# Performance work log

Hardware: AMD Instinct MI355X
Metric: run time of the kernel (lower is better)

Reference implementation:

```python
import jax, jax.numpy as jnp
import numpy as np

DIM = 512
NUM_HEADS = 8
HEAD_DIM = DIM // NUM_HEADS
EPS = 1e-6


def setup_inputs() -> dict:
    key = jax.random.key(0)
    k_x, k_qkv, k_out, k_b = jax.random.split(key, 4)
    B, N = 8, 4096
    x = jax.random.normal(k_x, (B, N, DIM), dtype=jnp.float32)
    # nn.Linear weights stored as [out_features, in_features]; we keep [in, out] for x @ W
    s_qkv = 1.0 / np.sqrt(DIM)
    W_qkv = jax.random.uniform(k_qkv, (DIM, 3 * DIM), minval=-s_qkv, maxval=s_qkv, dtype=jnp.float32)
    W_out = jax.random.uniform(k_out, (DIM, DIM), minval=-s_qkv, maxval=s_qkv, dtype=jnp.float32)
    b_out = jax.random.uniform(k_b, (DIM,), minval=-s_qkv, maxval=s_qkv, dtype=jnp.float32)
    return {"x": x, "W_qkv": W_qkv, "W_out": W_out, "b_out": b_out}


def _feature_map(x):
    # elu(x) + 1
    return jax.nn.elu(x) + 1.0


def reference(x, W_qkv, W_out, b_out):
    B, N, C = x.shape
    H, D = NUM_HEADS, HEAD_DIM
    qkv = x @ W_qkv                              # [B, N, 3C]
    qkv = qkv.reshape(B, N, 3, H, D).transpose(2, 0, 3, 1, 4)  # [3, B, H, N, D]
    q, k, v = qkv[0], qkv[1], qkv[2]
    q_phi = _feature_map(q)                      # [B, H, N, D]
    k_phi = _feature_map(k)
    KV = jnp.einsum('bhnd,bhne->bhde', k_phi, v)  # [B, H, D, D]
    K_sum = k_phi.sum(axis=2)                     # [B, H, D]
    denom = jnp.einsum('bhnd,bhd->bhn', q_phi, K_sum)[..., None] + EPS  # [B, H, N, 1]
    out = jnp.einsum('bhnd,bhde->bhne', q_phi, KV) / denom              # [B, H, N, D]
    out = out.transpose(0, 2, 1, 3).reshape(B, N, C)
    return out @ W_out + b_out
```

## Files before the change

### kernel.cpp

```cpp
#include <hip/hip_runtime.h>
#include <stdint.h>

typedef float    f32x4 __attribute__((ext_vector_type(4)));
typedef short    s16x8 __attribute__((ext_vector_type(8)));
typedef short    s16x4 __attribute__((ext_vector_type(4)));
typedef unsigned short u16;
typedef uint32_t u32;

#define DEVINL __device__ __forceinline__

DEVINL float bf2f(u16 u) { union { u32 i; float f; } x; x.i = ((u32)u) << 16; return x.f; }
DEVINL u16 f2bf(float f) {
  union { float f; u32 i; } x; x.f = f;
  u32 i = x.i;
  return (u16)((i + 0x7FFFu + ((i >> 16) & 1u)) >> 16);
}

DEVINL void gload16(const void* g, void* l) {
  __builtin_amdgcn_global_load_lds((const __attribute__((address_space(1))) void*)g,
                                   (__attribute__((address_space(3))) void*)l,
                                   16, 0, 0);
}

__global__ __launch_bounds__(256) void k_prep(const float* __restrict__ x,
                                              u16* __restrict__ xb,
                                              const float* __restrict__ Wqkv,
                                              u16* __restrict__ wqkvt,
                                              const float* __restrict__ Wout,
                                              u16* __restrict__ woutt) {
  __shared__ __align__(16) float t[64][65];
  int b = blockIdx.x;
  int tid = threadIdx.x;
  if (b < 2048) {
    const int n8 = 2097152;
    int stride = 2048 * 256;
    for (int i = b * 256 + tid; i < n8; i += stride) {
      const f32x4* p = (const f32x4*)(x + (size_t)i * 8);
      f32x4 a = p[0], c = p[1];
      s16x8 o;
      o[0] = (short)f2bf(a[0]); o[1] = (short)f2bf(a[1]);
      o[2] = (short)f2bf(a[2]); o[3] = (short)f2bf(a[3]);
      o[4] = (short)f2bf(c[0]); o[5] = (short)f2bf(c[1]);
      o[6] = (short)f2bf(c[2]); o[7] = (short)f2bf(c[3]);
      *(s16x8*)(xb + (size_t)i * 8) = o;
    }
    return;
  }
  const float* W; u16* Wt; int K, N, tb;
  if (b < 2048 + 192) { W = Wqkv; Wt = wqkvt; K = 512; N = 1536; tb = b - 2048; }
  else               { W = Wout; Wt = woutt; K = 512; N = 512;  tb = b - 2240; }
  int nb = N >> 6;
  int tn = tb % nb, tk = tb / nb;
  int n0 = tn << 6, k0 = tk << 6;
  int cr = tid >> 4, cc = (tid & 15) << 2;
#pragma unroll
  for (int i = 0; i < 4; i++) {
    int r = cr + (i << 4);
    f32x4 v = *(const f32x4*)(W + (size_t)(k0 + r) * N + n0 + cc);
    t[r][cc] = v[0]; t[r][cc + 1] = v[1]; t[r][cc + 2] = v[2]; t[r][cc + 3] = v[3];
  }
  __syncthreads();
#pragma unroll
  for (int i = 0; i < 4; i++) {
    int nn = cr + (i << 4);
    s16x4 o;
    o[0] = (short)f2bf(t[cc    ][nn]);
    o[1] = (short)f2bf(t[cc + 1][nn]);
    o[2] = (short)f2bf(t[cc + 2][nn]);
    o[3] = (short)f2bf(t[cc + 3][nn]);
    *(s16x4*)(Wt + (size_t)(n0 + nn) * K + k0 + cc) = o;
  }
}

__global__ __launch_bounds__(512, 1) void k_gemm1(
    const u16* __restrict__ A, const u16* __restrict__ Bt,
    u16* __restrict__ qph, u16* __restrict__ kphT, u16* __restrict__ vT) {
  __shared__ __align__(16) u16 lsA[3][256 * 32];
  __shared__ __align__(16) u16 lsB[3][256 * 32];
  const int nbn = 6;
  int nwg = gridDim.x;
  int bx = blockIdx.x;
  int o = (bx & 7) * (nwg >> 3) + (bx >> 3);
  int bm = o / nbn, bn = o % nbn;
  int m0 = bm << 8, n0 = bn << 8;
  int tid = threadIdx.x;
  int w = tid >> 6, lane = tid & 63;
  int lnlo = lane & 15, lnhi = lane >> 4;
  int wr = w >> 2, wc = w & 3;

  const u16* gAp[2]; const u16* gBp[2]; int ldst[2];
#pragma unroll
  for (int i = 0; i < 2; i++) {
    int c = tid + i * 512;
    int row = c >> 2, ch = c & 3;
    int gch = ch ^ ((row >> 1) & 3);
    gAp[i] = A + (size_t)(m0 + row) * 512 + gch * 8;
    gBp[i] = Bt + (size_t)(n0 + row) * 512 + gch * 8;
    ldst[i] = c * 8;
  }
  int offA[8], offB[4];
#pragma unroll
  for (int f = 0; f < 8; f++) {
    int r = wr * 128 + f * 16 + lnlo;
    offA[f] = r * 32 + (lnhi ^ ((r >> 1) & 3)) * 8;
  }
#pragma unroll
  for (int f = 0; f < 4; f++) {
    int r = wc * 64 + f * 16 + lnlo;
    offB[f] = r * 32 + (lnhi ^ ((r >> 1) & 3)) * 8;
  }

  f32x4 acc[8][4] = {};

#pragma unroll
  for (int i = 0; i < 2; i++) gload16(gAp[i], &lsA[0][ldst[i]]);
#pragma unroll
  for (int i = 0; i < 2; i++) gload16(gBp[i], &lsB[0][ldst[i]]);
#pragma unroll
  for (int i = 0; i < 2; i++) gload16(gAp[i] + 32, &lsA[1][ldst[i]]);
#pragma unroll
  for (int i = 0; i < 2; i++) gload16(gBp[i] + 32, &lsB[1][ldst[i]]);
  asm volatile("s_waitcnt vmcnt(4)" ::: "memory");
  __builtin_amdgcn_s_barrier();

#pragma unroll
  for (int t = 0; t < 16; t++) {
    int buf = t % 3;
    const u16* La = &lsA[buf][0];
    const u16* Lb = &lsB[buf][0];
    int k2 = (t + 2) * 32;
    int b2 = (t + 2) % 3;

    s16x8 bf[4], af[4];
#pragma unroll
    for (int f = 0; f < 4; f++) bf[f] = *(const s16x8*)(Lb + offB[f]);
#pragma unroll
    for (int f = 0; f < 4; f++) af[f] = *(const s16x8*)(La + offA[f]);
    if (t < 14) {
#pragma unroll
      for (int i = 0; i < 2; i++) gload16(gAp[i] + k2, &lsA[b2][ldst[i]]);
    }
    __builtin_amdgcn_s_barrier();
    __builtin_amdgcn_s_setprio(1);
#pragma unroll
    for (int mf = 0; mf < 4; mf++)
#pragma unroll
      for (int nf = 0; nf < 4; nf++)
        acc[mf][nf] = __builtin_amdgcn_mfma_f32_16x16x32_bf16(af[mf], bf[nf], acc[mf][nf], 0, 0, 0);
    __builtin_amdgcn_s_setprio(0);
    __builtin_amdgcn_s_barrier();

    s16x8 af2[4];
#pragma unroll
    for (int f = 0; f < 4; f++) af2[f] = *(const s16x8*)(La + offA[4 + f]);
    if (t < 14) {
#pragma unroll
      for (int i = 0; i < 2; i++) gload16(gBp[i] + k2, &lsB[b2][ldst[i]]);
    }
    __builtin_amdgcn_s_barrier();
    __builtin_amdgcn_s_setprio(1);
#pragma unroll
    for (int mf = 0; mf < 4; mf++)
#pragma unroll
      for (int nf = 0; nf < 4; nf++)
        acc[4 + mf][nf] = __builtin_amdgcn_mfma_f32_16x16x32_bf16(af2[mf], bf[nf], acc[4 + mf][nf], 0, 0, 0);
    __builtin_amdgcn_s_setprio(0);
    if (t <= 13)      asm volatile("s_waitcnt vmcnt(4)" ::: "memory");
    else if (t == 14) asm volatile("s_waitcnt vmcnt(0)" ::: "memory");
    if (t < 15) __builtin_amdgcn_s_barrier();
  }

  int gmB = m0 + wr * 128;
  int gnB = n0 + wc * 64;
  int sec = n0 >> 9;
  if (sec == 0) {
#pragma unroll
    for (int mf = 0; mf < 8; mf++) {
#pragma unroll
      for (int nf = 0; nf < 4; nf++) {
        int col = gnB + nf * 16 + lnlo;
        int hh = (col >> 6) & 7;
        int dd = col & 63;
#pragma unroll
        for (int r = 0; r < 4; r++) {
          int rowm = gmB + mf * 16 + lnhi * 4 + r;
          float val = acc[mf][nf][r];
          val = (val > 0.f) ? (val + 1.f) : __expf(val);
          int bidx = rowm >> 12, tok = rowm & 4095;
          qph[(((size_t)(bidx * 8 + hh) * 4096 + tok) << 6) + dd] = f2bf(val);
        }
      }
    }
  } else {
    u16* dstT = (sec == 1) ? kphT : vT;
    bool isphi = (sec == 1);
#pragma unroll
    for (int mf = 0; mf < 8; mf++) {
      int rowm = gmB + mf * 16 + lnhi * 4;
      int bidx = rowm >> 12, tok = rowm & 4095;
#pragma unroll
      for (int nf = 0; nf < 4; nf++) {
        int col = gnB + nf * 16 + lnlo;
        int hh = (col >> 6) & 7;
        int dd = col & 63;
        s16x4 o4;
#pragma unroll
        for (int r = 0; r < 4; r++) {
          float val = acc[mf][nf][r];
          if (isphi) val = (val > 0.f) ? (val + 1.f) : __expf(val);
          o4[r] = (short)f2bf(val);
        }
        *(s16x4*)&dstT[((size_t)(bidx * 8 + hh) * 64 + dd) * 4096 + tok] = o4;
      }
    }
  }
}

__global__ __launch_bounds__(256, 2) void k_kv(const u16* __restrict__ kphT,
                                               const u16* __restrict__ vT,
                                               float* __restrict__ kvpart,
                                               float* __restrict__ kspart) {
  __shared__ __align__(16) u16 lsK[64 * 256];
  __shared__ __align__(16) u16 lsV[64 * 256];
  __shared__ float red[4][64];
  int bx = blockIdx.x;
  int bh = bx >> 4, ck = bx & 15;
  int tid = threadIdx.x, w = tid >> 6, lane = tid & 63;
  int lnlo = lane & 15, lnhi = lane >> 4;
  size_t gbase = (size_t)bh * 64 * 4096 + ck * 256;

#pragma unroll
  for (int i = 0; i < 8; i++) {
    int c = tid + i * 256;
    int row = c >> 5, ch = c & 31;
    int gch = ch ^ (row & 31);
    gload16(kphT + gbase + (size_t)row * 4096 + gch * 8, &lsK[c * 8]);
  }
#pragma unroll
  for (int i = 0; i < 8; i++) {
    int c = tid + i * 256;
    int row = c >> 5, ch = c & 31;
    int gch = ch ^ (row & 31);
    gload16(vT + gbase + (size_t)row * 4096 + gch * 8, &lsV[c * 8]);
  }
  asm volatile("s_waitcnt vmcnt(0)" ::: "memory");
  __builtin_amdgcn_s_barrier();

  f32x4 acc[4] = {{0.f, 0.f, 0.f, 0.f}, {0.f, 0.f, 0.f, 0.f},
                  {0.f, 0.f, 0.f, 0.f}, {0.f, 0.f, 0.f, 0.f}};
  int rb = w * 16 + lnlo;
#pragma unroll
  for (int kk = 0; kk < 8; kk++) {
    s16x8 bfr = *(const s16x8*)&lsV[rb * 256 + ((kk * 4 + lnhi) ^ (rb & 31)) * 8];
#pragma unroll
    for (int mf = 0; mf < 4; mf++) {
      int ra = mf * 16 + lnlo;
      s16x8 af = *(const s16x8*)&lsK[ra * 256 + ((kk * 4 + lnhi) ^ (ra & 31)) * 8];
      acc[mf] = __builtin_amdgcn_mfma_f32_16x16x32_bf16(af, bfr, acc[mf], 0, 0, 0);
    }
  }

  {
    int d = tid & 63, q = tid >> 6;
    float s = 0.f;
#pragma unroll
    for (int j = 0; j < 8; j++) {
      s16x8 v8 = *(const s16x8*)&lsK[d * 256 + (q * 8 + j) * 8];
#pragma unroll
      for (int e = 0; e < 8; e++) s += bf2f((u16)v8[e]);
    }
    red[q][d] = s;
  }
  __syncthreads();

  size_t pb = (size_t)(bh * 16 + ck) * 4096;
#pragma unroll
  for (int mf = 0; mf < 4; mf++)
#pragma unroll
    for (int r = 0; r < 4; r++)
      kvpart[pb + (size_t)(mf * 16 + lnhi * 4 + r) * 64 + (w * 16 + lnlo)] = acc[mf][r];
  if (tid < 64)
    kspart[(size_t)(bh * 16 + ck) * 64 + tid] =
        red[0][tid] + red[1][tid] + red[2][tid] + red[3][tid];
}

__global__ __launch_bounds__(256) void k_w2(const float* __restrict__ kvpart,
                                            const float* __restrict__ kspart,
                                            const u16* __restrict__ woutt,
                                            const u16* __restrict__ qphi,
                                            u16* __restrict__ w2t,
                                            float* __restrict__ rdng) {
  __shared__ __align__(16) u16 kvls[64 * 64];
  __shared__ float ksumv[64];
  int blk = blockIdx.x, tid = threadIdx.x;
  if (blk < 64) {
    int bh = blk, b = bh >> 3, h = bh & 7;
    int w = tid >> 6, lane = tid & 63, lnlo = lane & 15, lnhi = lane >> 4;
    int d = tid >> 2, e0 = (tid & 3) << 4;
    size_t pb = (size_t)bh * 16 * 4096;
    f32x4 s0 = {}, s1 = {}, s2 = {}, s3 = {};
    for (int c = 0; c < 16; c++) {
      const float* p = kvpart + pb + (size_t)c * 4096 + d * 64 + e0;
      s0 += *(const f32x4*)(p);
      s1 += *(const f32x4*)(p + 4);
      s2 += *(const f32x4*)(p + 8);
      s3 += *(const f32x4*)(p + 12);
    }
    s16x8 o0, o1;
#pragma unroll
    for (int j = 0; j < 4; j++) {
      o0[j] = (short)f2bf(s0[j]); o0[4 + j] = (short)f2bf(s1[j]);
      o1[j] = (short)f2bf(s2[j]); o1[4 + j] = (short)f2bf(s3[j]);
    }
    int ch0 = e0 >> 3;
    *(s16x8*)&kvls[d * 64 + (ch0 ^ (d & 7)) * 8] = o0;
    *(s16x8*)&kvls[d * 64 + ((ch0 + 1) ^ (d & 7)) * 8] = o1;
    __syncthreads();
    f32x4 acc[4][8] = {};
#pragma unroll
    for (int kk = 0; kk < 2; kk++) {
      s16x8 af[4], bfr[8];
#pragma unroll
      for (int mf = 0; mf < 4; mf++) {
        int r = mf * 16 + lnlo;
        af[mf] = *(const s16x8*)&kvls[r * 64 + ((kk * 4 + lnhi) ^ (r & 7)) * 8];
      }
#pragma unroll
      for (int nf = 0; nf < 8; nf++) {
        int n = w * 128 + nf * 16 + lnlo;
        bfr[nf] = *(const s16x8*)&woutt[(size_t)n * 512 + h * 64 + (kk * 4 + lnhi) * 8];
      }
#pragma unroll
      for (int mf = 0; mf < 4; mf++)
#pragma unroll
        for (int nf = 0; nf < 8; nf++)
          acc[mf][nf] = __builtin_amdgcn_mfma_f32_16x16x32_bf16(af[mf], bfr[nf], acc[mf][nf], 0, 0, 0);
    }
#pragma unroll
    for (int mf = 0; mf < 4; mf++)
#pragma unroll
      for (int nf = 0; nf < 8; nf++) {
        int n = w * 128 + nf * 16 + lnlo;
        s16x4 o4;
#pragma unroll
        for (int r = 0; r < 4; r++) o4[r] = (short)f2bf(acc[mf][nf][r]);
        *(s16x4*)&w2t[(size_t)b * 262144 + (size_t)n * 512 + h * 64 + mf * 16 + lnhi * 4] = o4;
      }
  } else {
    int blk2 = blk - 64;
    int bh = blk2 >> 3, tch = blk2 & 7;
    if (tid < 64) {
      float s = 0.f;
#pragma unroll
      for (int c = 0; c < 16; c++) s += kspart[(size_t)bh * 1024 + c * 64 + tid];
      ksumv[tid] = s;
    }
    __syncthreads();
#pragma unroll
    for (int tt = 0; tt < 2; tt++) {
      int tok = tch * 512 + tid * 2 + tt;
      const u16* qp = qphi + ((size_t)bh * 4096 + tok) * 64;
      float den = 0.f;
#pragma unroll
      for (int cch = 0; cch < 8; cch++) {
        s16x8 v8 = *(const s16x8*)(qp + cch * 8);
        f32x4 k0 = *(const f32x4*)&ksumv[cch * 8];
        f32x4 k1 = *(const f32x4*)&ksumv[cch * 8 + 4];
#pragma unroll
        for (int j = 0; j < 4; j++) den += bf2f((u16)v8[j]) * k0[j];
#pragma unroll
        for (int j = 0; j < 4; j++) den += bf2f((u16)v8[4 + j]) * k1[j];
      }
      rdng[(size_t)bh * 4096 + tok] = 1.f / (den + 1e-6f);
    }
  }
}

__global__ __launch_bounds__(512, 1) void k_out(
    const u16* __restrict__ qphi, const u16* __restrict__ w2t,
    const float* __restrict__ rdng, const float* __restrict__ bias,
    float* __restrict__ out) {
  __shared__ __align__(16) u16 lsA[3][256 * 32];
  __shared__ __align__(16) u16 lsB[3][256 * 32];
  int nwg = gridDim.x, bx = blockIdx.x;
  int o = (bx & 7) * (nwg >> 3) + (bx >> 3);
  int bm = o >> 1, bn = o & 1;
  int m0 = bm << 8, n0 = bn << 8;
  int b = m0 >> 12;
  int tid = threadIdx.x, w = tid >> 6, lane = tid & 63;
  int lnlo = lane & 15, lnhi = lane >> 4;
  int wr = w >> 2, wc = w & 3;

  int ldst[2];
  const u16* qb_[2]; const u16* gB_[2]; const float* rb_[2];
#pragma unroll
  for (int i = 0; i < 2; i++) {
    int c = tid + i * 512, row = c >> 2, ch = c & 3;
    int gch = ch ^ ((row >> 1) & 3);
    int tok = (m0 + row) & 4095;
    qb_[i] = qphi + ((size_t)(b * 8) * 4096 + tok) * 64 + gch * 8;
    rb_[i] = rdng + (size_t)(b * 8) * 4096 + tok;
    gB_[i] = w2t + (size_t)b * 262144 + (size_t)(n0 + row) * 512 + gch * 8;
    ldst[i] = c * 8;
  }
  int offA[8], offB[4];
#pragma unroll
  for (int f = 0; f < 8; f++) {
    int r = wr * 128 + f * 16 + lnlo;
    offA[f] = r * 32 + (lnhi ^ ((r >> 1) & 3)) * 8;
  }
#pragma unroll
  for (int f = 0; f < 4; f++) {
    int r = wc * 64 + f * 16 + lnlo;
    offB[f] = r * 32 + (lnhi ^ ((r >> 1) & 3)) * 8;
  }

  f32x4 acc[8][4] = {};
  s16x8 ar[2]; float rr[2];

  auto loadA = [&](int t) {
#pragma unroll
    for (int i = 0; i < 2; i++) {
      ar[i] = *(const s16x8*)(qb_[i] + (size_t)(t >> 1) * 262144 + (t & 1) * 32);
      rr[i] = rb_[i][(size_t)(t >> 1) * 4096];
    }
  };
  auto writeA = [&](int buf) {
#pragma unroll
    for (int i = 0; i < 2; i++) {
      s16x8 oo;
#pragma unroll
      for (int j = 0; j < 8; j++) oo[j] = (short)f2bf(bf2f((u16)ar[i][j]) * rr[i]);
      *(s16x8*)&lsA[buf][ldst[i]] = oo;
    }
  };
  auto stageB = [&](int t) {
    int buf = t % 3;
#pragma unroll
    for (int i = 0; i < 2; i++) gload16(gB_[i] + t * 32, &lsB[buf][ldst[i]]);
  };

  loadA(0); writeA(0);
  loadA(1); writeA(1);
  stageB(0); stageB(1);
  asm volatile("s_waitcnt lgkmcnt(0)" ::: "memory");
  asm volatile("s_waitcnt vmcnt(2)" ::: "memory");
  __builtin_amdgcn_s_barrier();

#pragma unroll
  for (int t = 0; t < 16; t++) {
    int buf = t % 3;
    const u16* La = &lsA[buf][0];
    const u16* Lb = &lsB[buf][0];

    s16x8 bf[4], af[4];
#pragma unroll
    for (int f = 0; f < 4; f++) bf[f] = *(const s16x8*)(Lb + offB[f]);
#pragma unroll
    for (int f = 0; f < 4; f++) af[f] = *(const s16x8*)(La + offA[f]);
    if (t < 14) loadA(t + 2);
    __builtin_amdgcn_s_barrier();
    __builtin_amdgcn_s_setprio(1);
#pragma unroll
    for (int mf = 0; mf < 4; mf++)
#pragma unroll
      for (int nf = 0; nf < 4; nf++)
        acc[mf][nf] = __builtin_amdgcn_mfma_f32_16x16x32_bf16(af[mf], bf[nf], acc[mf][nf], 0, 0, 0);
    __builtin_amdgcn_s_setprio(0);
    __builtin_amdgcn_s_barrier();

    s16x8 af2[4];
#pragma unroll
    for (int f = 0; f < 4; f++) af2[f] = *(const s16x8*)(La + offA[4 + f]);
    if (t < 14) stageB(t + 2);
    __builtin_amdgcn_s_barrier();
    __builtin_amdgcn_s_setprio(1);
#pragma unroll
    for (int mf = 0; mf < 4; mf++)
#pragma unroll
      for (int nf = 0; nf < 4; nf++)
        acc[4 + mf][nf] = __builtin_amdgcn_mfma_f32_16x16x32_bf16(af2[mf], bf[nf], acc[4 + mf][nf], 0, 0, 0);
    __builtin_amdgcn_s_setprio(0);
    if (t < 14) writeA((t + 2) % 3);
    if (t == 14) asm volatile("s_waitcnt vmcnt(0)" ::: "memory");
    if (t < 15) {
      asm volatile("s_waitcnt lgkmcnt(0)" ::: "memory");
      __builtin_amdgcn_s_barrier();
    }
  }

  int gmB = m0 + wr * 128;
  int gnB = n0 + wc * 64;
#pragma unroll
  for (int mf = 0; mf < 8; mf++) {
#pragma unroll
    for (int nf = 0; nf < 4; nf++) {
      int col = gnB + nf * 16 + lnlo;
      float bv = bias[col];
#pragma unroll
      for (int r = 0; r < 4; r++) {
        int rowm = gmB + mf * 16 + lnhi * 4 + r;
        out[(size_t)rowm * 512 + col] = acc[mf][nf][r] + bv;
      }
    }
  }
}

#define OFF_XB     ((size_t)0)
#define OFF_W2T    ((size_t)0)
#define OFF_RDN    ((size_t)4194304)
#define OFF_WQKVT  ((size_t)33554432)
#define OFF_WOUTT  ((size_t)35127296)
#define OFF_QPHI   ((size_t)35651584)
#define OFF_KPHI   ((size_t)69206016)
#define OFF_VBUF   ((size_t)102760448)
#define OFF_KVPART ((size_t)136314880)
#define OFF_KSPART ((size_t)153092096)

extern "C" void kernel_launch(void* const* d_in, const int* in_sizes, int n_in,
                              void* d_out, int out_size, void* d_ws, size_t ws_size,
                              hipStream_t stream) {
  const float* x    = (const float*)d_in[0];
  const float* Wqkv = (const float*)d_in[1];
  const float* Wout = (const float*)d_in[2];
  const float* bout = (const float*)d_in[3];
  float* out = (float*)d_out;
  char* ws = (char*)d_ws;

  u16* xb     = (u16*)(ws + OFF_XB);
  u16* w2t    = (u16*)(ws + OFF_W2T);
  float* rdng = (float*)(ws + OFF_RDN);
  u16* wqkvt  = (u16*)(ws + OFF_WQKVT);
  u16* woutt  = (u16*)(ws + OFF_WOUTT);
  u16* qphi   = (u16*)(ws + OFF_QPHI);
  u16* kphT   = (u16*)(ws + OFF_KPHI);
  u16* vT     = (u16*)(ws + OFF_VBUF);
  float* kvpart = (float*)(ws + OFF_KVPART);
  float* kspart = (float*)(ws + OFF_KSPART);

  k_prep<<<2304, 256, 0, stream>>>(x, xb, Wqkv, wqkvt, Wout, woutt);
  k_gemm1<<<768, 512, 0, stream>>>(xb, wqkvt, qphi, kphT, vT);
  k_kv<<<1024, 256, 0, stream>>>(kphT, vT, kvpart, kspart);
  k_w2<<<576, 256, 0, stream>>>(kvpart, kspart, woutt, qphi, w2t, rdng);
  k_out<<<256, 512, 0, stream>>>(qphi, w2t, rdng, bout, out);
}
```

Baseline: 153.6 us.

## Shrink GEMM tiles to 128x128, double-buffer, prescale q by denominator

Both bf16 GEMMs move from 256x256 tiles with 512 threads and a triple-buffered split pipeline to 128x128 tiles with 256 threads, a simple double buffer and four blocks per CU. This gives more workgroups, so the CUs fill more evenly. The reciprocal denominator is now applied to q_phi inside k_w2, which writes a normalized bf16 copy into the freed k_phi buffer. k_out can then stream A directly into LDS with async loads instead of scaling it in registers. The trade-off is less data reuse per tile, an extra full read and write of q in k_w2, and a vmcnt(0) wait at every k-step.

```diff
diff --git a/kernel.cpp b/kernel.cpp
--- a/kernel.cpp
+++ b/kernel.cpp
@@ -72,75 +72,62 @@
   }
 }
 
-__global__ __launch_bounds__(512, 1) void k_gemm1(
+__global__ __launch_bounds__(256, 4) void k_g1(
     const u16* __restrict__ A, const u16* __restrict__ Bt,
     u16* __restrict__ qph, u16* __restrict__ kphT, u16* __restrict__ vT) {
-  __shared__ __align__(16) u16 lsA[3][256 * 32];
-  __shared__ __align__(16) u16 lsB[3][256 * 32];
-  const int nbn = 6;
-  int nwg = gridDim.x;
-  int bx = blockIdx.x;
+  __shared__ __align__(16) u16 lsA[2][128 * 32];
+  __shared__ __align__(16) u16 lsB[2][128 * 32];
+  const int nbn = 12;
+  int nwg = gridDim.x, bx = blockIdx.x;
   int o = (bx & 7) * (nwg >> 3) + (bx >> 3);
   int bm = o / nbn, bn = o % nbn;
-  int m0 = bm << 8, n0 = bn << 8;
-  int tid = threadIdx.x;
-  int w = tid >> 6, lane = tid & 63;
+  int m0 = bm << 7, n0 = bn << 7;
+  int tid = threadIdx.x, w = tid >> 6, lane = tid & 63;
   int lnlo = lane & 15, lnhi = lane >> 4;
-  int wr = w >> 2, wc = w & 3;
+  int wr = w >> 1, wc = w & 1;
 
   const u16* gAp[2]; const u16* gBp[2]; int ldst[2];
 #pragma unroll
   for (int i = 0; i < 2; i++) {
-    int c = tid + i * 512;
-    int row = c >> 2, ch = c & 3;
+    int c = tid + i * 256, row = c >> 2, ch = c & 3;
     int gch = ch ^ ((row >> 1) & 3);
     gAp[i] = A + (size_t)(m0 + row) * 512 + gch * 8;
     gBp[i] = Bt + (size_t)(n0 + row) * 512 + gch * 8;
     ldst[i] = c * 8;
   }
-  int offA[8], offB[4];
-#pragma unroll
-  for (int f = 0; f < 8; f++) {
-    int r = wr * 128 + f * 16 + lnlo;
-    offA[f] = r * 32 + (lnhi ^ ((r >> 1) & 3)) * 8;
-  }
+  int offA[4], offB[4];
 #pragma unroll
   for (int f = 0; f < 4; f++) {
-    int r = wc * 64 + f * 16 + lnlo;
-    offB[f] = r * 32 + (lnhi ^ ((r >> 1) & 3)) * 8;
-  }
-
-  f32x4 acc[8][4] = {};
+    int rA = wr * 64 + f * 16 + lnlo;
+    offA[f] = rA * 32 + (lnhi ^ ((rA >> 1) & 3)) * 8;
+    int rB = wc * 64 + f * 16 + lnlo;
+    offB[f] = rB * 32 + (lnhi ^ ((rB >> 1) & 3)) * 8;
+  }
+
+  f32x4 acc[4][4] = {};
 
 #pragma unroll
   for (int i = 0; i < 2; i++) gload16(gAp[i], &lsA[0][ldst[i]]);
 #pragma unroll
   for (int i = 0; i < 2; i++) gload16(gBp[i], &lsB[0][ldst[i]]);
-#pragma unroll
-  for (int i = 0; i < 2; i++) gload16(gAp[i] + 32, &lsA[1][ldst[i]]);
-#pragma unroll
-  for (int i = 0; i < 2; i++) gload16(gBp[i] + 32, &lsB[1][ldst[i]]);
-  asm volatile("s_waitcnt vmcnt(4)" ::: "memory");
+  asm volatile("s_waitcnt vmcnt(0)" ::: "memory");
   __builtin_amdgcn_s_barrier();
 
 #pragma unroll
   for (int t = 0; t < 16; t++) {
-    int buf = t % 3;
-    const u16* La = &lsA[buf][0];
-    const u16* Lb = &lsB[buf][0];
-    int k2 = (t + 2) * 32;
-    int b2 = (t + 2) % 3;
-
-    s16x8 bf[4], af[4];
-#pragma unroll
-    for (int f = 0; f < 4; f++) bf[f] = *(const s16x8*)(Lb + offB[f]);
-#pragma unroll
-    for (int f = 0; f < 4; f++) af[f] = *(const s16x8*)(La + offA[f]);
-    if (t < 14) {
-#pragma unroll
-      for (int i = 0; i < 2; i++) gload16(gAp[i] + k2, &lsA[b2][ldst[i]]);
-    }
-    __builtin_amdgcn_s_barrier();
+    int par = t & 1;
+    if (t < 15) {
+      int k1 = (t + 1) * 32;
+#pragma unroll
+      for (int i = 0; i < 2; i++) gload16(gAp[i] + k1, &lsA[par ^ 1][ldst[i]]);
+#pragma unroll
+      for (int i = 0; i < 2; i++) gload16(gBp[i] + k1, &lsB[par ^ 1][ldst[i]]);
+    }
+    s16x8 af[4], bf[4];
+#pragma unroll
+    for (int f = 0; f < 4; f++) af[f] = *(const s16x8*)&lsA[par][offA[f]];
+#pragma unroll
+    for (int f = 0; f < 4; f++) bf[f] = *(const s16x8*)&lsB[par][offB[f]];
     __builtin_amdgcn_s_setprio(1);
 #pragma unroll
     for (int mf = 0; mf < 4; mf++)
@@ -148,34 +135,18 @@
       for (int nf = 0; nf < 4; nf++)
         acc[mf][nf] = __builtin_amdgcn_mfma_f32_16x16x32_bf16(af[mf], bf[nf], acc[mf][nf], 0, 0, 0);
     __builtin_amdgcn_s_setprio(0);
-    __builtin_amdgcn_s_barrier();
-
-    s16x8 af2[4];
-#pragma unroll
-    for (int f = 0; f < 4; f++) af2[f] = *(const s16x8*)(La + offA[4 + f]);
-    if (t < 14) {
-#pragma unroll
-      for (int i = 0; i < 2; i++) gload16(gBp[i] + k2, &lsB[b2][ldst[i]]);
-    }
-    __builtin_amdgcn_s_barrier();
-    __builtin_amdgcn_s_setprio(1);
-#pragma unroll
-    for (int mf = 0; mf < 4; mf++)
-#pragma unroll
-      for (int nf = 0; nf < 4; nf++)
-        acc[4 + mf][nf] = __builtin_amdgcn_mfma_f32_16x16x32_bf16(af2[mf], bf[nf], acc[4 + mf][nf], 0, 0, 0);
-    __builtin_amdgcn_s_setprio(0);
-    if (t <= 13)      asm volatile("s_waitcnt vmcnt(4)" ::: "memory");
-    else if (t == 14) asm volatile("s_waitcnt vmcnt(0)" ::: "memory");
-    if (t < 15) __builtin_amdgcn_s_barrier();
-  }
-
-  int gmB = m0 + wr * 128;
+    if (t < 15) {
+      asm volatile("s_waitcnt vmcnt(0)" ::: "memory");
+      __builtin_amdgcn_s_barrier();
+    }
+  }
+
+  int gmB = m0 + wr * 64;
   int gnB = n0 + wc * 64;
   int sec = n0 >> 9;
   if (sec == 0) {
 #pragma unroll
-    for (int mf = 0; mf < 8; mf++) {
+    for (int mf = 0; mf < 4; mf++) {
 #pragma unroll
       for (int nf = 0; nf < 4; nf++) {
         int col = gnB + nf * 16 + lnlo;
@@ -195,7 +166,7 @@
     u16* dstT = (sec == 1) ? kphT : vT;
     bool isphi = (sec == 1);
 #pragma unroll
-    for (int mf = 0; mf < 8; mf++) {
+    for (int mf = 0; mf < 4; mf++) {
       int rowm = gmB + mf * 16 + lnhi * 4;
       int bidx = rowm >> 12, tok = rowm & 4095;
 #pragma unroll
@@ -289,7 +260,7 @@
                                             const u16* __restrict__ woutt,
                                             const u16* __restrict__ qphi,
                                             u16* __restrict__ w2t,
-                                            float* __restrict__ rdng) {
+                                            u16* __restrict__ qphs) {
   __shared__ __align__(16) u16 kvls[64 * 64];
   __shared__ float ksumv[64];
   int blk = blockIdx.x, tid = threadIdx.x;
@@ -358,108 +329,90 @@
     __syncthreads();
 #pragma unroll
     for (int tt = 0; tt < 2; tt++) {
-      int tok = tch * 512 + tid * 2 + tt;
+      int tok = tch * 512 + tt * 256 + tid;
       const u16* qp = qphi + ((size_t)bh * 4096 + tok) * 64;
+      s16x8 v8[8];
       float den = 0.f;
 #pragma unroll
       for (int cch = 0; cch < 8; cch++) {
-        s16x8 v8 = *(const s16x8*)(qp + cch * 8);
-        f32x4 k0 = *(const f32x4*)&ksumv[cch * 8];
-        f32x4 k1 = *(const f32x4*)&ksumv[cch * 8 + 4];
-#pragma unroll
-        for (int j = 0; j < 4; j++) den += bf2f((u16)v8[j]) * k0[j];
-#pragma unroll
-        for (int j = 0; j < 4; j++) den += bf2f((u16)v8[4 + j]) * k1[j];
-      }
-      rdng[(size_t)bh * 4096 + tok] = 1.f / (den + 1e-6f);
-    }
-  }
-}
-
-__global__ __launch_bounds__(512, 1) void k_out(
-    const u16* __restrict__ qphi, const u16* __restrict__ w2t,
-    const float* __restrict__ rdng, const float* __restrict__ bias,
-    float* __restrict__ out) {
-  __shared__ __align__(16) u16 lsA[3][256 * 32];
-  __shared__ __align__(16) u16 lsB[3][256 * 32];
+        v8[cch] = *(const s16x8*)(qp + cch * 8);
+#pragma unroll
+        for (int j = 0; j < 8; j++) den += bf2f((u16)v8[cch][j]) * ksumv[cch * 8 + j];
+      }
+      float rdn = 1.f / (den + 1e-6f);
+      u16* qd = qphs + ((size_t)bh * 4096 + tok) * 64;
+#pragma unroll
+      for (int cch = 0; cch < 8; cch++) {
+        s16x8 oo;
+#pragma unroll
+        for (int j = 0; j < 8; j++) oo[j] = (short)f2bf(bf2f((u16)v8[cch][j]) * rdn);
+        *(s16x8*)(qd + cch * 8) = oo;
+      }
+    }
+  }
+}
+
+__global__ __launch_bounds__(256, 4) void k_out(
+    const u16* __restrict__ qphs, const u16* __restrict__ w2t,
+    const float* __restrict__ bias, float* __restrict__ out) {
+  __shared__ __align__(16) u16 lsA[2][128 * 32];
+  __shared__ __align__(16) u16 lsB[2][128 * 32];
+  const int nbn = 4;
   int nwg = gridDim.x, bx = blockIdx.x;
   int o = (bx & 7) * (nwg >> 3) + (bx >> 3);
-  int bm = o >> 1, bn = o & 1;
-  int m0 = bm << 8, n0 = bn << 8;
+  int bm = o / nbn, bn = o % nbn;
+  int m0 = bm << 7, n0 = bn << 7;
   int b = m0 >> 12;
   int tid = threadIdx.x, w = tid >> 6, lane = tid & 63;
   int lnlo = lane & 15, lnhi = lane >> 4;
-  int wr = w >> 2, wc = w & 3;
-
-  int ldst[2];
-  const u16* qb_[2]; const u16* gB_[2]; const float* rb_[2];
+  int wr = w >> 1, wc = w & 1;
+
+  const u16* qb_[2]; const u16* gBp[2]; int ldst[2];
 #pragma unroll
   for (int i = 0; i < 2; i++) {
-    int c = tid + i * 512, row = c >> 2, ch = c & 3;
+    int c = tid + i * 256, row = c >> 2, ch = c & 3;
     int gch = ch ^ ((row >> 1) & 3);
     int tok = (m0 + row) & 4095;
-    qb_[i] = qphi + ((size_t)(b * 8) * 4096 + tok) * 64 + gch * 8;
-    rb_[i] = rdng + (size_t)(b * 8) * 4096 + tok;
-    gB_[i] = w2t + (size_t)b * 262144 + (size_t)(n0 + row) * 512 + gch * 8;
+    qb_[i] = qphs + ((size_t)(b * 8) * 4096 + tok) * 64 + gch * 8;
+    gBp[i] = w2t + (size_t)b * 262144 + (size_t)(n0 + row) * 512 + gch * 8;
     ldst[i] = c * 8;
   }
-  int offA[8], offB[4];
-#pragma unroll
-  for (int f = 0; f < 8; f++) {
-    int r = wr * 128 + f * 16 + lnlo;
-    offA[f] = r * 32 + (lnhi ^ ((r >> 1) & 3)) * 8;
-  }
+  int offA[4], offB[4];
 #pragma unroll
   for (int f = 0; f < 4; f++) {
-    int r = wc * 64 + f * 16 + lnlo;
-    offB[f] = r * 32 + (lnhi ^ ((r >> 1) & 3)) * 8;
-  }
-
-  f32x4 acc[8][4] = {};
-  s16x8 ar[2]; float rr[2];
-
-  auto loadA = [&](int t) {
-#pragma unroll
-    for (int i = 0; i < 2; i++) {
-      ar[i] = *(const s16x8*)(qb_[i] + (size_t)(t >> 1) * 262144 + (t & 1) * 32);
-      rr[i] = rb_[i][(size_t)(t >> 1) * 4096];
-    }
+    int rA = wr * 64 + f * 16 + lnlo;
+    offA[f] = rA * 32 + (lnhi ^ ((rA >> 1) & 3)) * 8;
+    int rB = wc * 64 + f * 16 + lnlo;
+    offB[f] = rB * 32 + (lnhi ^ ((rB >> 1) & 3)) * 8;
+  }
+
+  f32x4 acc[4][4] = {};
+
+  auto stageA = [&](int t, int buf) {
+    size_t hoff = (size_t)(t >> 1) * 262144 + (t & 1) * 32;
+#pragma unroll
+    for (int i = 0; i < 2; i++) gload16(qb_[i] + hoff, &lsA[buf][ldst[i]]);
   };
-  auto writeA = [&](int buf) {
-#pragma unroll
-    for (int i = 0; i < 2; i++) {
-      s16x8 oo;
-#pragma unroll
-      for (int j = 0; j < 8; j++) oo[j] = (short)f2bf(bf2f((u16)ar[i][j]) * rr[i]);
-      *(s16x8*)&lsA[buf][ldst[i]] = oo;
-    }
-  };
-  auto stageB = [&](int t) {
-    int buf = t % 3;
-#pragma unroll
-    for (int i = 0; i < 2; i++) gload16(gB_[i] + t * 32, &lsB[buf][ldst[i]]);
-  };
-
-  loadA(0); writeA(0);
-  loadA(1); writeA(1);
-  stageB(0); stageB(1);
-  asm volatile("s_waitcnt lgkmcnt(0)" ::: "memory");
-  asm volatile("s_waitcnt vmcnt(2)" ::: "memory");
+#pragma unroll
+  for (int i = 0; i < 2; i++) gload16(gBp[i], &lsB[0][ldst[i]]);
+  stageA(0, 0);
+  asm volatile("s_waitcnt vmcnt(0)" ::: "memory");
   __builtin_amdgcn_s_barrier();
 
 #pragma unroll
   for (int t = 0; t < 16; t++) {
-    int buf = t % 3;
-    const u16* La = &lsA[buf][0];
-    const u16* Lb = &lsB[buf][0];
-
-    s16x8 bf[4], af[4];
-#pragma unroll
-    for (int f = 0; f < 4; f++) bf[f] = *(const s16x8*)(Lb + offB[f]);
-#pragma unroll
-    for (int f = 0; f < 4; f++) af[f] = *(const s16x8*)(La + offA[f]);
-    if (t < 14) loadA(t + 2);
-    __builtin_amdgcn_s_barrier();
+    int par = t & 1;
+    if (t < 15) {
+      int k1 = (t + 1) * 32;
+      stageA(t + 1, par ^ 1);
+#pragma unroll
+      for (int i = 0; i < 2; i++) gload16(gBp[i] + k1, &lsB[par ^ 1][ldst[i]]);
+    }
+    s16x8 af[4], bf[4];
+#pragma unroll
+    for (int f = 0; f < 4; f++) af[f] = *(const s16x8*)&lsA[par][offA[f]];
+#pragma unroll
+    for (int f = 0; f < 4; f++) bf[f] = *(const s16x8*)&lsB[par][offB[f]];
     __builtin_amdgcn_s_setprio(1);
 #pragma unroll
     for (int mf = 0; mf < 4; mf++)
@@ -467,32 +420,16 @@
       for (int nf = 0; nf < 4; nf++)
         acc[mf][nf] = __builtin_amdgcn_mfma_f32_16x16x32_bf16(af[mf], bf[nf], acc[mf][nf], 0, 0, 0);
     __builtin_amdgcn_s_setprio(0);
-    __builtin_amdgcn_s_barrier();
-
-    s16x8 af2[4];
-#pragma unroll
-    for (int f = 0; f < 4; f++) af2[f] = *(const s16x8*)(La + offA[4 + f]);
-    if (t < 14) stageB(t + 2);
-    __builtin_amdgcn_s_barrier();
-    __builtin_amdgcn_s_setprio(1);
-#pragma unroll
-    for (int mf = 0; mf < 4; mf++)
-#pragma unroll
-      for (int nf = 0; nf < 4; nf++)
-        acc[4 + mf][nf] = __builtin_amdgcn_mfma_f32_16x16x32_bf16(af2[mf], bf[nf], acc[4 + mf][nf], 0, 0, 0);
-    __builtin_amdgcn_s_setprio(0);
-    if (t < 14) writeA((t + 2) % 3);
-    if (t == 14) asm volatile("s_waitcnt vmcnt(0)" ::: "memory");
     if (t < 15) {
-      asm volatile("s_waitcnt lgkmcnt(0)" ::: "memory");
+      asm volatile("s_waitcnt vmcnt(0)" ::: "memory");
       __builtin_amdgcn_s_barrier();
     }
   }
 
-  int gmB = m0 + wr * 128;
+  int gmB = m0 + wr * 64;
   int gnB = n0 + wc * 64;
 #pragma unroll
-  for (int mf = 0; mf < 8; mf++) {
+  for (int mf = 0; mf < 4; mf++) {
 #pragma unroll
     for (int nf = 0; nf < 4; nf++) {
       int col = gnB + nf * 16 + lnlo;
@@ -508,7 +445,6 @@
 
 #define OFF_XB     ((size_t)0)
 #define OFF_W2T    ((size_t)0)
-#define OFF_RDN    ((size_t)4194304)
 #define OFF_WQKVT  ((size_t)33554432)
 #define OFF_WOUTT  ((size_t)35127296)
 #define OFF_QPHI   ((size_t)35651584)
@@ -529,18 +465,18 @@
 
   u16* xb     = (u16*)(ws + OFF_XB);
   u16* w2t    = (u16*)(ws + OFF_W2T);
-  float* rdng = (float*)(ws + OFF_RDN);
   u16* wqkvt  = (u16*)(ws + OFF_WQKVT);
   u16* woutt  = (u16*)(ws + OFF_WOUTT);
   u16* qphi   = (u16*)(ws + OFF_QPHI);
   u16* kphT   = (u16*)(ws + OFF_KPHI);
+  u16* qphs   = (u16*)(ws + OFF_KPHI);
   u16* vT     = (u16*)(ws + OFF_VBUF);
   float* kvpart = (float*)(ws + OFF_KVPART);
   float* kspart = (float*)(ws + OFF_KSPART);
 
   k_prep<<<2304, 256, 0, stream>>>(x, xb, Wqkv, wqkvt, Wout, woutt);
-  k_gemm1<<<768, 512, 0, stream>>>(xb, wqkvt, qphi, kphT, vT);
+  k_g1<<<3072, 256, 0, stream>>>(xb, wqkvt, qphi, kphT, vT);
   k_kv<<<1024, 256, 0, stream>>>(kphT, vT, kvpart, kspart);
-  k_w2<<<576, 256, 0, stream>>>(kvpart, kspart, woutt, qphi, w2t, rdng);
-  k_out<<<256, 512, 0, stream>>>(qphi, w2t, rdng, bout, out);
-}
+  k_w2<<<576, 256, 0, stream>>>(kvpart, kspart, woutt, qphi, w2t, qphs);
+  k_out<<<1024, 256, 0, stream>>>(qphs, w2t, bout, out);
+}
```

Result: slower. 162.9 us (+6.1%).

## Pre-scale q_phi by reciprocal denominator in k_w2 and DMA A tiles in k_out

Applied to the files above, without the earlier changes.

The denominator kernel now multiplies q_phi by 1/denom and writes a pre-scaled bf16 copy into the dead k_phi buffer. k_out can then stage the A operand with direct global-to-LDS loads like B, instead of register loads, a per-element multiply and LDS writes. This removes VALU work and LDS store traffic from the GEMM main loop and simplifies its waits. The cost is an extra 32MB write and read pass in k_w2, and the token mapping changes to a coalesced stride.

```diff
diff --git a/kernel.cpp b/kernel.cpp
--- a/kernel.cpp
+++ b/kernel.cpp
@@ -289,7 +289,7 @@
                                             const u16* __restrict__ woutt,
                                             const u16* __restrict__ qphi,
                                             u16* __restrict__ w2t,
-                                            float* __restrict__ rdng) {
+                                            u16* __restrict__ qphs) {
   __shared__ __align__(16) u16 kvls[64 * 64];
   __shared__ float ksumv[64];
   int blk = blockIdx.x, tid = threadIdx.x;
@@ -358,49 +358,52 @@
     __syncthreads();
 #pragma unroll
     for (int tt = 0; tt < 2; tt++) {
-      int tok = tch * 512 + tid * 2 + tt;
+      int tok = tch * 512 + tt * 256 + tid;
       const u16* qp = qphi + ((size_t)bh * 4096 + tok) * 64;
+      s16x8 v8[8];
       float den = 0.f;
 #pragma unroll
       for (int cch = 0; cch < 8; cch++) {
-        s16x8 v8 = *(const s16x8*)(qp + cch * 8);
-        f32x4 k0 = *(const f32x4*)&ksumv[cch * 8];
-        f32x4 k1 = *(const f32x4*)&ksumv[cch * 8 + 4];
-#pragma unroll
-        for (int j = 0; j < 4; j++) den += bf2f((u16)v8[j]) * k0[j];
-#pragma unroll
-        for (int j = 0; j < 4; j++) den += bf2f((u16)v8[4 + j]) * k1[j];
-      }
-      rdng[(size_t)bh * 4096 + tok] = 1.f / (den + 1e-6f);
+        v8[cch] = *(const s16x8*)(qp + cch * 8);
+#pragma unroll
+        for (int j = 0; j < 8; j++) den += bf2f((u16)v8[cch][j]) * ksumv[cch * 8 + j];
+      }
+      float rdn = 1.f / (den + 1e-6f);
+      u16* qd = qphs + ((size_t)bh * 4096 + tok) * 64;
+#pragma unroll
+      for (int cch = 0; cch < 8; cch++) {
+        s16x8 oo;
+#pragma unroll
+        for (int j = 0; j < 8; j++) oo[j] = (short)f2bf(bf2f((u16)v8[cch][j]) * rdn);
+        *(s16x8*)(qd + cch * 8) = oo;
+      }
     }
   }
 }
 
 __global__ __launch_bounds__(512, 1) void k_out(
-    const u16* __restrict__ qphi, const u16* __restrict__ w2t,
-    const float* __restrict__ rdng, const float* __restrict__ bias,
-    float* __restrict__ out) {
+    const u16* __restrict__ qphs, const u16* __restrict__ w2t,
+    const float* __restrict__ bias, float* __restrict__ out) {
   __shared__ __align__(16) u16 lsA[3][256 * 32];
   __shared__ __align__(16) u16 lsB[3][256 * 32];
+  const int nbn = 2;
   int nwg = gridDim.x, bx = blockIdx.x;
   int o = (bx & 7) * (nwg >> 3) + (bx >> 3);
-  int bm = o >> 1, bn = o & 1;
+  int bm = o / nbn, bn = o % nbn;
   int m0 = bm << 8, n0 = bn << 8;
   int b = m0 >> 12;
   int tid = threadIdx.x, w = tid >> 6, lane = tid & 63;
   int lnlo = lane & 15, lnhi = lane >> 4;
   int wr = w >> 2, wc = w & 3;
 
-  int ldst[2];
-  const u16* qb_[2]; const u16* gB_[2]; const float* rb_[2];
+  const u16* qb_[2]; const u16* gBp[2]; int ldst[2];
 #pragma unroll
   for (int i = 0; i < 2; i++) {
     int c = tid + i * 512, row = c >> 2, ch = c & 3;
     int gch = ch ^ ((row >> 1) & 3);
     int tok = (m0 + row) & 4095;
-    qb_[i] = qphi + ((size_t)(b * 8) * 4096 + tok) * 64 + gch * 8;
-    rb_[i] = rdng + (size_t)(b * 8) * 4096 + tok;
-    gB_[i] = w2t + (size_t)b * 262144 + (size_t)(n0 + row) * 512 + gch * 8;
+    qb_[i] = qphs + ((size_t)(b * 8) * 4096 + tok) * 64 + gch * 8;
+    gBp[i] = w2t + (size_t)b * 262144 + (size_t)(n0 + row) * 512 + gch * 8;
     ldst[i] = c * 8;
   }
   int offA[8], offB[4];
@@ -416,35 +419,20 @@
   }
 
   f32x4 acc[8][4] = {};
-  s16x8 ar[2]; float rr[2];
-
-  auto loadA = [&](int t) {
-#pragma unroll
-    for (int i = 0; i < 2; i++) {
-      ar[i] = *(const s16x8*)(qb_[i] + (size_t)(t >> 1) * 262144 + (t & 1) * 32);
-      rr[i] = rb_[i][(size_t)(t >> 1) * 4096];
-    }
+
+  auto stageA = [&](int t, int buf) {
+    size_t hoff = (size_t)(t >> 1) * 262144 + (t & 1) * 32;
+#pragma unroll
+    for (int i = 0; i < 2; i++) gload16(qb_[i] + hoff, &lsA[buf][ldst[i]]);
   };
-  auto writeA = [&](int buf) {
-#pragma unroll
-    for (int i = 0; i < 2; i++) {
-      s16x8 oo;
-#pragma unroll
-      for (int j = 0; j < 8; j++) oo[j] = (short)f2bf(bf2f((u16)ar[i][j]) * rr[i]);
-      *(s16x8*)&lsA[buf][ldst[i]] = oo;
-    }
+  auto stageB = [&](int t, int buf) {
+#pragma unroll
+    for (int i = 0; i < 2; i++) gload16(gBp[i] + t * 32, &lsB[buf][ldst[i]]);
   };
-  auto stageB = [&](int t) {
-    int buf = t % 3;
-#pragma unroll
-    for (int i = 0; i < 2; i++) gload16(gB_[i] + t * 32, &lsB[buf][ldst[i]]);
-  };
-
-  loadA(0); writeA(0);
-  loadA(1); writeA(1);
-  stageB(0); stageB(1);
-  asm volatile("s_waitcnt lgkmcnt(0)" ::: "memory");
-  asm volatile("s_waitcnt vmcnt(2)" ::: "memory");
+
+  stageA(0, 0); stageB(0, 0);
+  stageA(1, 1); stageB(1, 1);
+  asm volatile("s_waitcnt vmcnt(4)" ::: "memory");
   __builtin_amdgcn_s_barrier();
 
 #pragma unroll
@@ -452,13 +440,14 @@
     int buf = t % 3;
     const u16* La = &lsA[buf][0];
     const u16* Lb = &lsB[buf][0];
+    int b2 = (t + 2) % 3;
 
     s16x8 bf[4], af[4];
 #pragma unroll
     for (int f = 0; f < 4; f++) bf[f] = *(const s16x8*)(Lb + offB[f]);
 #pragma unroll
     for (int f = 0; f < 4; f++) af[f] = *(const s16x8*)(La + offA[f]);
-    if (t < 14) loadA(t + 2);
+    if (t < 14) stageA(t + 2, b2);
     __builtin_amdgcn_s_barrier();
     __builtin_amdgcn_s_setprio(1);
 #pragma unroll
@@ -472,7 +461,7 @@
     s16x8 af2[4];
 #pragma unroll
     for (int f = 0; f < 4; f++) af2[f] = *(const s16x8*)(La + offA[4 + f]);
-    if (t < 14) stageB(t + 2);
+    if (t < 14) stageB(t + 2, b2);
     __builtin_amdgcn_s_barrier();
     __builtin_amdgcn_s_setprio(1);
 #pragma unroll
@@ -481,12 +470,9 @@
       for (int nf = 0; nf < 4; nf++)
         acc[4 + mf][nf] = __builtin_amdgcn_mfma_f32_16x16x32_bf16(af2[mf], bf[nf], acc[4 + mf][nf], 0, 0, 0);
     __builtin_amdgcn_s_setprio(0);
-    if (t < 14) writeA((t + 2) % 3);
-    if (t == 14) asm volatile("s_waitcnt vmcnt(0)" ::: "memory");
-    if (t < 15) {
-      asm volatile("s_waitcnt lgkmcnt(0)" ::: "memory");
-      __builtin_amdgcn_s_barrier();
-    }
+    if (t <= 13)      asm volatile("s_waitcnt vmcnt(4)" ::: "memory");
+    else if (t == 14) asm volatile("s_waitcnt vmcnt(0)" ::: "memory");
+    if (t < 15) __builtin_amdgcn_s_barrier();
   }
 
   int gmB = m0 + wr * 128;
@@ -508,7 +494,6 @@
 
 #define OFF_XB     ((size_t)0)
 #define OFF_W2T    ((size_t)0)
-#define OFF_RDN    ((size_t)4194304)
 #define OFF_WQKVT  ((size_t)33554432)
 #define OFF_WOUTT  ((size_t)35127296)
 #define OFF_QPHI   ((size_t)35651584)
@@ -529,11 +514,11 @@
 
   u16* xb     = (u16*)(ws + OFF_XB);
   u16* w2t    = (u16*)(ws + OFF_W2T);
-  float* rdng = (float*)(ws + OFF_RDN);
   u16* wqkvt  = (u16*)(ws + OFF_WQKVT);
   u16* woutt  = (u16*)(ws + OFF_WOUTT);
   u16* qphi   = (u16*)(ws + OFF_QPHI);
   u16* kphT   = (u16*)(ws + OFF_KPHI);
+  u16* qphs   = (u16*)(ws + OFF_KPHI);
   u16* vT     = (u16*)(ws + OFF_VBUF);
   float* kvpart = (float*)(ws + OFF_KVPART);
   float* kspart = (float*)(ws + OFF_KSPART);
@@ -541,6 +526,6 @@
   k_prep<<<2304, 256, 0, stream>>>(x, xb, Wqkv, wqkvt, Wout, woutt);
   k_gemm1<<<768, 512, 0, stream>>>(xb, wqkvt, qphi, kphT, vT);
   k_kv<<<1024, 256, 0, stream>>>(kphT, vT, kvpart, kspart);
-  k_w2<<<576, 256, 0, stream>>>(kvpart, kspart, woutt, qphi, w2t, rdng);
-  k_out<<<256, 512, 0, stream>>>(qphi, w2t, rdng, bout, out);
-}
+  k_w2<<<576, 256, 0, stream>>>(kvpart, kspart, woutt, qphi, w2t, qphs);
+  k_out<<<256, 512, 0, stream>>>(qphs, w2t, bout, out);
+}
```

New measurement: 157.5 us. 2.6% more time.
